# Optimization experiments

Measured on AMD Instinct MI355X. Metric: run time of the kernel, lower is better.

## Reference

```python
import jax, jax.numpy as jnp
import numpy as np

D_MODEL = 1024
NUM_HEADS = 16
D_FF = 4096
EPS = 1e-5


def setup_inputs() -> dict:
    key = jax.random.key(0)
    ks = jax.random.split(key, 8)
    B, S, D = 4, 2048, D_MODEL
    s = 1.0 / np.sqrt(D)
    return {
        "x": jax.random.normal(ks[0], (B, S, D), jnp.float32),
        "ln1_w": jnp.ones((D,), jnp.float32),
        "ln2_w": jnp.ones((D,), jnp.float32),
        "wq": jax.random.normal(ks[1], (D, D), jnp.float32) * s,
        "wk": jax.random.normal(ks[2], (D, D), jnp.float32) * s,
        "wv": jax.random.normal(ks[3], (D, D), jnp.float32) * s,
        "wo": jax.random.normal(ks[4], (D, D), jnp.float32) * s,
        "w1": jax.random.normal(ks[5], (D_FF, D), jnp.float32) * s,
        "w2": jax.random.normal(ks[6], (D, D_FF), jnp.float32) * (1.0 / np.sqrt(D_FF)),
    }


def rmsnorm(a, w):
    # (a * w) / sqrt(mean(a^2) + eps)  -- matches torch module exactly
    denom = jnp.sqrt(jnp.mean(jnp.square(a), axis=-1, keepdims=True) + EPS)
    return a * w / denom


def attention(x, wq, wk, wv, wo):
    B, S, D = x.shape
    H, dk = NUM_HEADS, D // NUM_HEADS
    q = (x @ wq.T).reshape(B, S, H, dk).transpose(0, 2, 1, 3)  # B H S dk
    k = (x @ wk.T).reshape(B, S, H, dk).transpose(0, 2, 1, 3)
    v = (x @ wv.T).reshape(B, S, H, dk).transpose(0, 2, 1, 3)
    scores = jnp.einsum("bhqd,bhkd->bhqk", q, k) / np.sqrt(dk)
    causal = jnp.triu(jnp.ones((S, S), bool), k=1)
    scores = jnp.where(causal, -jnp.inf, scores)
    probs = jax.nn.softmax(scores, axis=-1)
    out = jnp.einsum("bhqk,bhkd->bhqd", probs, v)
    out = out.transpose(0, 2, 1, 3).reshape(B, S, D)
    return out @ wo.T


def ffn(x, w1, w2):
    h = x @ w1.T
    h = 0.5 * h * (1.0 + jax.lax.erf(h / np.sqrt(2.0).astype(np.float32)))
    return h @ w2.T


def reference(x, ln1_w, ln2_w, wq, wk, wv, wo, w1, w2):
    y = x + attention(rmsnorm(x, ln1_w), wq, wk, wv, wo)
    return y + ffn(rmsnorm(y, ln2_w), w1, w2)
```

## Files before the change

### kernel.cpp

```cpp
#include <hip/hip_runtime.h>

#define DM    1024
#define DFF   4096
#define SEQ   2048
#define BATCH 4
#define NROWS (BATCH * SEQ)
#define HEADS 16
#define DKH   64
#define KSTR  (2 * DM)

typedef __attribute__((ext_vector_type(4))) float          f32x4;
typedef __attribute__((ext_vector_type(8))) __bf16         bf16x8;
typedef __attribute__((ext_vector_type(8))) unsigned short u16x8;
typedef __attribute__((ext_vector_type(4))) unsigned short u16x4;

static __device__ __forceinline__ unsigned short f2bf(float f) {
  unsigned u = __builtin_bit_cast(unsigned, f);
  u += 0x7fffu + ((u >> 16) & 1u);
  return (unsigned short)(u >> 16);
}

__global__ void k_f2bf(const float* __restrict__ in, unsigned short* __restrict__ out, int n4) {
  int i = blockIdx.x * blockDim.x + threadIdx.x;
  if (i >= n4) return;
  float4 v = reinterpret_cast<const float4*>(in)[i];
  ushort4 o;
  o.x = f2bf(v.x); o.y = f2bf(v.y); o.z = f2bf(v.z); o.w = f2bf(v.w);
  reinterpret_cast<ushort4*>(out)[i] = o;
}

__global__ __launch_bounds__(256) void k_rmsnorm(const float* __restrict__ x,
                                                 const float* __restrict__ w,
                                                 unsigned short* __restrict__ out) {
  const int row = blockIdx.x;
  const float4 v = reinterpret_cast<const float4*>(x + (size_t)row * DM)[threadIdx.x];
  float ss = v.x * v.x + v.y * v.y + v.z * v.z + v.w * v.w;
#pragma unroll
  for (int off = 32; off > 0; off >>= 1) ss += __shfl_down(ss, off);
  __shared__ float red[4];
  if ((threadIdx.x & 63) == 0) red[threadIdx.x >> 6] = ss;
  __syncthreads();
  const float tot  = red[0] + red[1] + red[2] + red[3];
  const float rden = rsqrtf(tot * (1.0f / DM) + 1e-5f);
  const float4 wv = reinterpret_cast<const float4*>(w)[threadIdx.x];
  ushort4 o;
  o.x = f2bf(v.x * wv.x * rden);
  o.y = f2bf(v.y * wv.y * rden);
  o.z = f2bf(v.z * wv.z * rden);
  o.w = f2bf(v.w * wv.w * rden);
  reinterpret_cast<ushort4*>(out + (size_t)row * DM)[threadIdx.x] = o;
}

template <int EPI>
__global__ __launch_bounds__(256) void k_gemm_nt(const unsigned short* __restrict__ A,
                                                 const unsigned short* __restrict__ B,
                                                 void* __restrict__ Cv,
                                                 const float* __restrict__ res,
                                                 int M, int N, int K) {
  alignas(16) __shared__ unsigned short As[2][128 * 32];
  alignas(16) __shared__ unsigned short Bs[2][128 * 32];
  const int t  = threadIdx.x;
  const int w  = t >> 6;
  const int l  = t & 63;
  const int wr = w >> 1, wc = w & 1;
  const int lr = l & 15, lk = l >> 4;

  const unsigned bid = blockIdx.y * gridDim.x + blockIdx.x;
  const unsigned cpx = (gridDim.x * gridDim.y) >> 3;
  const unsigned sw  = (bid & 7) * cpx + (bid >> 3);
  const int m0 = (int)(sw / gridDim.x) * 128;
  const int n0 = (int)(sw % gridDim.x) * 128;

  const int srow = t >> 2;
  const int sgr  = (t & 3) ^ (srow & 3);

  auto stage = [&](int buf, int k0) {
#pragma unroll
    for (int r = 0; r < 2; ++r) {
      const unsigned short* ga = A + (size_t)(m0 + r * 64 + srow) * K + k0 + 8 * sgr;
      const unsigned short* gb = B + (size_t)(n0 + r * 64 + srow) * K + k0 + 8 * sgr;
      __builtin_amdgcn_global_load_lds((__attribute__((address_space(1))) void*)ga,
                                       (__attribute__((address_space(3))) void*)(&As[buf][r * 2048 + w * 512]),
                                       16, 0, 0);
      __builtin_amdgcn_global_load_lds((__attribute__((address_space(1))) void*)gb,
                                       (__attribute__((address_space(3))) void*)(&Bs[buf][r * 2048 + w * 512]),
                                       16, 0, 0);
    }
  };

  f32x4 acc[4][4] = {};

  stage(0, 0);
  const int nIt = K >> 5;
  for (int it = 0; it < nIt; ++it) {
    const int buf = it & 1;
    __syncthreads();
    if (it + 1 < nIt) stage(buf ^ 1, (it + 1) << 5);

    bf16x8 af[4], bf[4];
#pragma unroll
    for (int m = 0; m < 4; ++m)
      af[m] = *reinterpret_cast<const bf16x8*>(
          &As[buf][(wr * 64 + m * 16 + lr) * 32 + 8 * (lk ^ (lr & 3))]);
#pragma unroll
    for (int n = 0; n < 4; ++n)
      bf[n] = *reinterpret_cast<const bf16x8*>(
          &Bs[buf][(wc * 64 + n * 16 + lr) * 32 + 8 * (lk ^ (lr & 3))]);
#pragma unroll
    for (int m = 0; m < 4; ++m)
#pragma unroll
      for (int n = 0; n < 4; ++n)
        acc[m][n] = __builtin_amdgcn_mfma_f32_16x16x32_bf16(af[m], bf[n], acc[m][n], 0, 0, 0);
  }

#pragma unroll
  for (int m = 0; m < 4; ++m) {
#pragma unroll
    for (int n = 0; n < 4; ++n) {
#pragma unroll
      for (int r = 0; r < 4; ++r) {
        const size_t row = (size_t)(m0 + wr * 64 + m * 16 + lk * 4 + r);
        const size_t col = (size_t)(n0 + wc * 64 + n * 16 + lr);
        const float a = acc[m][n][r];
        if constexpr (EPI == 0) {
          ((unsigned short*)Cv)[row * N + col] = f2bf(a);
        } else if constexpr (EPI == 1) {
          ((float*)Cv)[row * N + col] = a + res[row * N + col];
        } else {
          const float h2 = a * a;
          const float e  = exp2f(a * (2.30221535f + 0.10295355f * h2));
          const float g  = a - a / (e + 1.0f);
          ((unsigned short*)Cv)[row * N + col] = f2bf(g);
        }
      }
    }
  }
}

__global__ __launch_bounds__(256, 2) void k_attn(const unsigned short* __restrict__ QK,
                                                 const unsigned short* __restrict__ VT,
                                                 unsigned short* __restrict__ O) {
  const int qtA = blockIdx.y & 7;
  const int qtB = (int)(SEQ / 128) - 1 - qtA;
  const int h   = blockIdx.x + 8 * (blockIdx.y >> 3);
  const int b   = blockIdx.z;
  const int t  = threadIdx.x, w = t >> 6, l = t & 63;
  const int lr = l & 15, lk = l >> 4;
  const size_t rowB = (size_t)b * SEQ;
  const int hoff  = h * DKH;
  const int qw2[2] = { qtA * 128 + 32 * w, qtB * 128 + 32 * w };

  alignas(16) __shared__ unsigned short Ks[2][64 * 64];
  alignas(16) __shared__ unsigned short Vt[2][64 * 64];
  alignas(16) __shared__ unsigned short Ps[2][4][32 * 64];

  char* const KsB = (char*)Ks;
  char* const VtB = (char*)Vt;

  auto stage = [&](int buf, int kb2) {
#pragma unroll
    for (int half = 0; half < 2; ++half) {
      const int srow = w * 16 + half * 8 + (l >> 3);
      const int sgr  = (l & 7) ^ (srow & 7);
      const unsigned short* gk = QK + (size_t)(rowB + kb2 + srow) * KSTR + DM + hoff + 8 * sgr;
      __builtin_amdgcn_global_load_lds((__attribute__((address_space(1))) void*)gk,
                                       (__attribute__((address_space(3))) void*)(KsB + buf * 8192 + w * 2048 + half * 1024),
                                       16, 0, 0);
      const unsigned short* gv = VT + (size_t)(hoff + srow) * NROWS + rowB + kb2 + 8 * sgr;
      __builtin_amdgcn_global_load_lds((__attribute__((address_space(1))) void*)gv,
                                       (__attribute__((address_space(3))) void*)(VtB + buf * 8192 + w * 2048 + half * 1024),
                                       16, 0, 0);
    }
  };

  bf16x8 qf[2][2][2];
#pragma unroll
  for (int s = 0; s < 2; ++s)
#pragma unroll
    for (int g = 0; g < 2; ++g)
#pragma unroll
      for (int kk = 0; kk < 2; ++kk)
        qf[s][g][kk] = *reinterpret_cast<const bf16x8*>(
            QK + (rowB + qw2[s] + 16 * g + lr) * KSTR + hoff + 32 * kk + 8 * lk);

  f32x4 oacc[2][2][4] = {};
  float mrun[2][2] = {{-1e30f, -1e30f}, {-1e30f, -1e30f}};
  float lrun[2][2] = {{0.0f, 0.0f}, {0.0f, 0.0f}};

  const float SCL = 0.18033688011f;

  const int ktmax = (qtB * 128 + 127) >> 6;
  stage(0, 0);
  for (int kt = 0; kt <= ktmax; ++kt) {
    const int kbase = kt * 64;
    const int cur   = kt & 1;
    __syncthreads();
    if (kt < ktmax) stage(cur ^ 1, kbase + 64);
    const char* Kc = KsB + cur * 8192;
    const char* Vc = VtB + cur * 8192;

    const bool act[2] = { kbase <= qw2[0] + 31, kbase <= qw2[1] + 31 };

    f32x4 sacc[2][2][4] = {};
#pragma unroll
    for (int tt = 0; tt < 4; ++tt) {
      bf16x8 kf0 = *reinterpret_cast<const bf16x8*>(Kc + (16 * tt + lr) * 128 + 16 * ((lk + 0) ^ (lr & 7)));
      bf16x8 kf1 = *reinterpret_cast<const bf16x8*>(Kc + (16 * tt + lr) * 128 + 16 * ((lk + 4) ^ (lr & 7)));
#pragma unroll
      for (int s = 0; s < 2; ++s) {
        if (!act[s]) continue;
#pragma unroll
        for (int g = 0; g < 2; ++g) {
          sacc[s][g][tt] = __builtin_amdgcn_mfma_f32_16x16x32_bf16(kf0, qf[s][g][0], sacc[s][g][tt], 0, 0, 0);
          sacc[s][g][tt] = __builtin_amdgcn_mfma_f32_16x16x32_bf16(kf1, qf[s][g][1], sacc[s][g][tt], 0, 0, 0);
        }
      }
    }

#pragma unroll
    for (int s = 0; s < 2; ++s) {
      if (!act[s]) continue;
      const int qw = qw2[s];
      char* const PsSB = (char*)(Ps[s][w]);
#pragma unroll
      for (int g = 0; g < 2; ++g) {
        const int qg = qw + 16 * g + lr;
        float sv[4][4];
        if (kbase + 63 > qw + 16 * g) {
#pragma unroll
          for (int tt = 0; tt < 4; ++tt)
#pragma unroll
            for (int r = 0; r < 4; ++r) {
              const int kg = kbase + 16 * tt + 4 * lk + r;
              sv[tt][r] = (kg > qg) ? -1e30f : sacc[s][g][tt][r] * SCL;
            }
        } else {
#pragma unroll
          for (int tt = 0; tt < 4; ++tt)
#pragma unroll
            for (int r = 0; r < 4; ++r) sv[tt][r] = sacc[s][g][tt][r] * SCL;
        }
        float tm = sv[0][0];
#pragma unroll
        for (int tt = 0; tt < 4; ++tt)
#pragma unroll
          for (int r = 0; r < 4; ++r) tm = fmaxf(tm, sv[tt][r]);
        tm = fmaxf(tm, __shfl_xor(tm, 16));
        tm = fmaxf(tm, __shfl_xor(tm, 32));
        float mref = mrun[s][g];
        if (__any(tm > mref + 8.0f)) {
          const float mnew  = fmaxf(mref, tm);
          const float alpha = exp2f(mref - mnew);
#pragma unroll
          for (int r = 0; r < 4; ++r) {
            const float ar = __shfl(alpha, 4 * lk + r);
#pragma unroll
            for (int dn = 0; dn < 4; ++dn) oacc[s][g][dn][r] *= ar;
          }
          lrun[s][g] *= alpha;
          mrun[s][g] = mnew;
          mref = mnew;
        }
        float ts = 0.0f;
        unsigned short pb[4][4];
#pragma unroll
        for (int tt = 0; tt < 4; ++tt)
#pragma unroll
          for (int r = 0; r < 4; ++r) {
            const float p = exp2f(sv[tt][r] - mref);
            ts += p;
            pb[tt][r] = __builtin_bit_cast(unsigned short, static_cast<__bf16>(p));
          }
        ts += __shfl_xor(ts, 16);
        ts += __shfl_xor(ts, 32);
        lrun[s][g] += ts;
#pragma unroll
        for (int tt = 0; tt < 4; ++tt) {
          u16x4 pw = {pb[tt][0], pb[tt][1], pb[tt][2], pb[tt][3]};
          *reinterpret_cast<u16x4*>(
              PsSB + (16 * g + lr) * 128 + ((32 * tt + 8 * lk) ^ (16 * (lr & 7)))) = pw;
        }
      }
    }

    asm volatile("" ::: "memory");

#pragma unroll
    for (int kk = 0; kk < 2; ++kk) {
      bf16x8 vf[4];
#pragma unroll
      for (int dn = 0; dn < 4; ++dn)
        vf[dn] = *reinterpret_cast<const bf16x8*>(
            Vc + (16 * dn + lr) * 128 + 16 * ((4 * kk + lk) ^ (lr & 7)));
#pragma unroll
      for (int s = 0; s < 2; ++s) {
        if (!act[s]) continue;
        char* const PsSB = (char*)(Ps[s][w]);
        bf16x8 pa[2];
#pragma unroll
        for (int g = 0; g < 2; ++g)
          pa[g] = *reinterpret_cast<const bf16x8*>(
              PsSB + (16 * g + lr) * 128 + ((64 * kk + 16 * lk) ^ (16 * (lr & 7))));
#pragma unroll
        for (int dn = 0; dn < 4; ++dn) {
          oacc[s][0][dn] = __builtin_amdgcn_mfma_f32_16x16x32_bf16(pa[0], vf[dn], oacc[s][0][dn], 0, 0, 0);
          oacc[s][1][dn] = __builtin_amdgcn_mfma_f32_16x16x32_bf16(pa[1], vf[dn], oacc[s][1][dn], 0, 0, 0);
        }
      }
    }

    asm volatile("" ::: "memory");
  }

#pragma unroll
  for (int s = 0; s < 2; ++s)
#pragma unroll
    for (int g = 0; g < 2; ++g)
#pragma unroll
      for (int r = 0; r < 4; ++r) {
        const float li = 1.0f / __shfl(lrun[s][g], 4 * lk + r);
        const size_t row = rowB + qw2[s] + 16 * g + 4 * lk + r;
#pragma unroll
        for (int dn = 0; dn < 4; ++dn)
          O[row * DM + hoff + 16 * dn + lr] = f2bf(oacc[s][g][dn][r] * li);
      }
}

extern "C" void kernel_launch(void* const* d_in, const int* in_sizes, int n_in,
                              void* d_out, int out_size, void* d_ws, size_t ws_size,
                              hipStream_t stream) {
  const float* x   = (const float*)d_in[0];
  const float* ln1 = (const float*)d_in[1];
  const float* ln2 = (const float*)d_in[2];
  const float* wq  = (const float*)d_in[3];
  const float* wk  = (const float*)d_in[4];
  const float* wv  = (const float*)d_in[5];
  const float* wo  = (const float*)d_in[6];
  const float* w1  = (const float*)d_in[7];
  const float* w2  = (const float*)d_in[8];

  char* ws = (char*)d_ws;
  size_t off = 0;
  auto take = [&](size_t bytes) { void* p = ws + off; off += bytes; return p; };
  unsigned short* wqkb = (unsigned short*)take((size_t)2 * DM * DM * 2);
  unsigned short* wvb  = (unsigned short*)take((size_t)DM * DM * 2);
  unsigned short* wob  = (unsigned short*)take((size_t)DM * DM * 2);
  unsigned short* w1b  = (unsigned short*)take((size_t)DFF * DM * 2);
  unsigned short* w2b  = (unsigned short*)take((size_t)DM * DFF * 2);
  unsigned short* qk   = (unsigned short*)take((size_t)NROWS * 2 * DM * 2);
  unsigned short* xn   = (unsigned short*)take((size_t)NROWS * DM * 2);
  unsigned short* vtb  = (unsigned short*)take((size_t)DM * NROWS * 2);
  float*          yb   = (float*)take((size_t)NROWS * DM * 4);
  unsigned short* hb   = (unsigned short*)take((size_t)NROWS * DFF * 2);
  unsigned short* yn   = qk;

  auto cvt = [&](const float* src, unsigned short* dst, size_t n) {
    int n4 = (int)(n / 4);
    k_f2bf<<<dim3((n4 + 255) / 256), dim3(256), 0, stream>>>(src, dst, n4);
  };
  cvt(wq, wqkb, (size_t)DM * DM);
  cvt(wk, wqkb + (size_t)DM * DM, (size_t)DM * DM);
  cvt(wv, wvb, (size_t)DM * DM);
  cvt(wo, wob, (size_t)DM * DM);
  cvt(w1, w1b, (size_t)DFF * DM);
  cvt(w2, w2b, (size_t)DM * DFF);

  k_rmsnorm<<<dim3(NROWS), dim3(256), 0, stream>>>(x, ln1, xn);

  k_gemm_nt<0><<<dim3(2 * DM / 128, NROWS / 128), dim3(256), 0, stream>>>(
      xn, wqkb, qk, nullptr, NROWS, 2 * DM, DM);

  k_gemm_nt<0><<<dim3(NROWS / 128, DM / 128), dim3(256), 0, stream>>>(
      wvb, xn, vtb, nullptr, DM, NROWS, DM);

  k_attn<<<dim3(SEQ / 256, HEADS, BATCH), dim3(256), 0, stream>>>(qk, vtb, xn);

  const dim3 gD(DM / 128, NROWS / 128);
  k_gemm_nt<1><<<gD, dim3(256), 0, stream>>>(xn, wob, yb, x, NROWS, DM, DM);

  k_rmsnorm<<<dim3(NROWS), dim3(256), 0, stream>>>(yb, ln2, yn);

  k_gemm_nt<2><<<dim3(DFF / 128, NROWS / 128), dim3(256), 0, stream>>>(yn, w1b, hb, nullptr, NROWS, DFF, DM);
  k_gemm_nt<1><<<gD, dim3(256), 0, stream>>>(hb, w2b, (float*)d_out, yb, NROWS, DM, DFF);
}
```

Before: 434.5 us.

## Halve attention query tile per wave and fold softmax scale into Q projection

The attention kernel now gives each wave 16 query rows per tile instead of 32, using 64-row tile pairs. This doubles the grid to 16x16x4 blocks and raises launch bounds to 3 blocks per CU, for more parallelism and finer causal load balance. The softmax scale (1/sqrt(dk)·log2e) is folded into the Q half of the QK projection epilogue, which removes a multiply per score. In exchange, each K/V tile staged in shared memory is reused by fewer queries, so K/V global traffic rises. Q is also rounded to bf16 after scaling, which slightly changes numerics.

```diff
diff --git a/kernel.cpp b/kernel.cpp
--- a/kernel.cpp
+++ b/kernel.cpp
@@ -126,33 +126,36 @@
           ((unsigned short*)Cv)[row * N + col] = f2bf(a);
         } else if constexpr (EPI == 1) {
           ((float*)Cv)[row * N + col] = a + res[row * N + col];
-        } else {
+        } else if constexpr (EPI == 2) {
           const float h2 = a * a;
           const float e  = exp2f(a * (2.30221535f + 0.10295355f * h2));
           const float g  = a - a / (e + 1.0f);
           ((unsigned short*)Cv)[row * N + col] = f2bf(g);
+        } else {
+          const float sc = (col < DM) ? 0.18033688011f : 1.0f;
+          ((unsigned short*)Cv)[row * N + col] = f2bf(a * sc);
         }
       }
     }
   }
 }
 
-__global__ __launch_bounds__(256, 2) void k_attn(const unsigned short* __restrict__ QK,
+__global__ __launch_bounds__(256, 3) void k_attn(const unsigned short* __restrict__ QK,
                                                  const unsigned short* __restrict__ VT,
                                                  unsigned short* __restrict__ O) {
-  const int qtA = blockIdx.y & 7;
-  const int qtB = (int)(SEQ / 128) - 1 - qtA;
-  const int h   = blockIdx.x + 8 * (blockIdx.y >> 3);
+  const int h   = blockIdx.x;
+  const int qtA = blockIdx.y;
+  const int qtB = 31 - qtA;
   const int b   = blockIdx.z;
   const int t  = threadIdx.x, w = t >> 6, l = t & 63;
   const int lr = l & 15, lk = l >> 4;
   const size_t rowB = (size_t)b * SEQ;
   const int hoff  = h * DKH;
-  const int qw2[2] = { qtA * 128 + 32 * w, qtB * 128 + 32 * w };
+  const int qw2[2] = { qtA * 64 + 16 * w, qtB * 64 + 16 * w };
 
   alignas(16) __shared__ unsigned short Ks[2][64 * 64];
   alignas(16) __shared__ unsigned short Vt[2][64 * 64];
-  alignas(16) __shared__ unsigned short Ps[2][4][32 * 64];
+  alignas(16) __shared__ unsigned short Ps[2][4][16 * 64];
 
   char* const KsB = (char*)Ks;
   char* const VtB = (char*)Vt;
@@ -173,23 +176,19 @@
     }
   };
 
-  bf16x8 qf[2][2][2];
+  bf16x8 qf[2][2];
 #pragma unroll
   for (int s = 0; s < 2; ++s)
 #pragma unroll
-    for (int g = 0; g < 2; ++g)
-#pragma unroll
-      for (int kk = 0; kk < 2; ++kk)
-        qf[s][g][kk] = *reinterpret_cast<const bf16x8*>(
-            QK + (rowB + qw2[s] + 16 * g + lr) * KSTR + hoff + 32 * kk + 8 * lk);
-
-  f32x4 oacc[2][2][4] = {};
-  float mrun[2][2] = {{-1e30f, -1e30f}, {-1e30f, -1e30f}};
-  float lrun[2][2] = {{0.0f, 0.0f}, {0.0f, 0.0f}};
-
-  const float SCL = 0.18033688011f;
-
-  const int ktmax = (qtB * 128 + 127) >> 6;
+    for (int kk = 0; kk < 2; ++kk)
+      qf[s][kk] = *reinterpret_cast<const bf16x8*>(
+          QK + (rowB + qw2[s] + lr) * KSTR + hoff + 32 * kk + 8 * lk);
+
+  f32x4 oacc[2][4] = {};
+  float mrun[2] = {-1e30f, -1e30f};
+  float lrun[2] = {0.0f, 0.0f};
+
+  const int ktmax = qtB;
   stage(0, 0);
   for (int kt = 0; kt <= ktmax; ++kt) {
     const int kbase = kt * 64;
@@ -199,9 +198,9 @@
     const char* Kc = KsB + cur * 8192;
     const char* Vc = VtB + cur * 8192;
 
-    const bool act[2] = { kbase <= qw2[0] + 31, kbase <= qw2[1] + 31 };
-
-    f32x4 sacc[2][2][4] = {};
+    const bool act[2] = { kbase <= qw2[0] + 15, kbase <= qw2[1] + 15 };
+
+    f32x4 sacc[2][4] = {};
 #pragma unroll
     for (int tt = 0; tt < 4; ++tt) {
       bf16x8 kf0 = *reinterpret_cast<const bf16x8*>(Kc + (16 * tt + lr) * 128 + 16 * ((lk + 0) ^ (lr & 7)));
@@ -209,11 +208,8 @@
 #pragma unroll
       for (int s = 0; s < 2; ++s) {
         if (!act[s]) continue;
-#pragma unroll
-        for (int g = 0; g < 2; ++g) {
-          sacc[s][g][tt] = __builtin_amdgcn_mfma_f32_16x16x32_bf16(kf0, qf[s][g][0], sacc[s][g][tt], 0, 0, 0);
-          sacc[s][g][tt] = __builtin_amdgcn_mfma_f32_16x16x32_bf16(kf1, qf[s][g][1], sacc[s][g][tt], 0, 0, 0);
-        }
+        sacc[s][tt] = __builtin_amdgcn_mfma_f32_16x16x32_bf16(kf0, qf[s][0], sacc[s][tt], 0, 0, 0);
+        sacc[s][tt] = __builtin_amdgcn_mfma_f32_16x16x32_bf16(kf1, qf[s][1], sacc[s][tt], 0, 0, 0);
       }
     }
 
@@ -222,64 +218,61 @@
       if (!act[s]) continue;
       const int qw = qw2[s];
       char* const PsSB = (char*)(Ps[s][w]);
-#pragma unroll
-      for (int g = 0; g < 2; ++g) {
-        const int qg = qw + 16 * g + lr;
-        float sv[4][4];
-        if (kbase + 63 > qw + 16 * g) {
-#pragma unroll
-          for (int tt = 0; tt < 4; ++tt)
-#pragma unroll
-            for (int r = 0; r < 4; ++r) {
-              const int kg = kbase + 16 * tt + 4 * lk + r;
-              sv[tt][r] = (kg > qg) ? -1e30f : sacc[s][g][tt][r] * SCL;
-            }
-        } else {
-#pragma unroll
-          for (int tt = 0; tt < 4; ++tt)
-#pragma unroll
-            for (int r = 0; r < 4; ++r) sv[tt][r] = sacc[s][g][tt][r] * SCL;
+      const int qg = qw + lr;
+      float sv[4][4];
+      if (kbase + 63 > qw) {
+#pragma unroll
+        for (int tt = 0; tt < 4; ++tt)
+#pragma unroll
+          for (int r = 0; r < 4; ++r) {
+            const int kg = kbase + 16 * tt + 4 * lk + r;
+            sv[tt][r] = (kg > qg) ? -1e30f : sacc[s][tt][r];
+          }
+      } else {
+#pragma unroll
+        for (int tt = 0; tt < 4; ++tt)
+#pragma unroll
+          for (int r = 0; r < 4; ++r) sv[tt][r] = sacc[s][tt][r];
+      }
+      float tm = sv[0][0];
+#pragma unroll
+      for (int tt = 0; tt < 4; ++tt)
+#pragma unroll
+        for (int r = 0; r < 4; ++r) tm = fmaxf(tm, sv[tt][r]);
+      tm = fmaxf(tm, __shfl_xor(tm, 16));
+      tm = fmaxf(tm, __shfl_xor(tm, 32));
+      float mref = mrun[s];
+      if (__any(tm > mref + 8.0f)) {
+        const float mnew  = fmaxf(mref, tm);
+        const float alpha = exp2f(mref - mnew);
+#pragma unroll
+        for (int r = 0; r < 4; ++r) {
+          const float ar = __shfl(alpha, 4 * lk + r);
+#pragma unroll
+          for (int dn = 0; dn < 4; ++dn) oacc[s][dn][r] *= ar;
         }
-        float tm = sv[0][0];
-#pragma unroll
-        for (int tt = 0; tt < 4; ++tt)
-#pragma unroll
-          for (int r = 0; r < 4; ++r) tm = fmaxf(tm, sv[tt][r]);
-        tm = fmaxf(tm, __shfl_xor(tm, 16));
-        tm = fmaxf(tm, __shfl_xor(tm, 32));
-        float mref = mrun[s][g];
-        if (__any(tm > mref + 8.0f)) {
-          const float mnew  = fmaxf(mref, tm);
-          const float alpha = exp2f(mref - mnew);
-#pragma unroll
-          for (int r = 0; r < 4; ++r) {
-            const float ar = __shfl(alpha, 4 * lk + r);
-#pragma unroll
-            for (int dn = 0; dn < 4; ++dn) oacc[s][g][dn][r] *= ar;
-          }
-          lrun[s][g] *= alpha;
-          mrun[s][g] = mnew;
-          mref = mnew;
+        lrun[s] *= alpha;
+        mrun[s] = mnew;
+        mref = mnew;
+      }
+      float ts = 0.0f;
+      unsigned short pb[4][4];
+#pragma unroll
+      for (int tt = 0; tt < 4; ++tt)
+#pragma unroll
+        for (int r = 0; r < 4; ++r) {
+          const float p = exp2f(sv[tt][r] - mref);
+          ts += p;
+          pb[tt][r] = __builtin_bit_cast(unsigned short, static_cast<__bf16>(p));
         }
-        float ts = 0.0f;
-        unsigned short pb[4][4];
-#pragma unroll
-        for (int tt = 0; tt < 4; ++tt)
-#pragma unroll
-          for (int r = 0; r < 4; ++r) {
-            const float p = exp2f(sv[tt][r] - mref);
-            ts += p;
-            pb[tt][r] = __builtin_bit_cast(unsigned short, static_cast<__bf16>(p));
-          }
-        ts += __shfl_xor(ts, 16);
-        ts += __shfl_xor(ts, 32);
-        lrun[s][g] += ts;
-#pragma unroll
-        for (int tt = 0; tt < 4; ++tt) {
-          u16x4 pw = {pb[tt][0], pb[tt][1], pb[tt][2], pb[tt][3]};
-          *reinterpret_cast<u16x4*>(
-              PsSB + (16 * g + lr) * 128 + ((32 * tt + 8 * lk) ^ (16 * (lr & 7)))) = pw;
-        }
+      ts += __shfl_xor(ts, 16);
+      ts += __shfl_xor(ts, 32);
+      lrun[s] += ts;
+#pragma unroll
+      for (int tt = 0; tt < 4; ++tt) {
+        u16x4 pw = {pb[tt][0], pb[tt][1], pb[tt][2], pb[tt][3]};
+        *reinterpret_cast<u16x4*>(
+            PsSB + lr * 128 + ((32 * tt + 8 * lk) ^ (16 * (lr & 7)))) = pw;
       }
     }
 
@@ -296,16 +289,11 @@
       for (int s = 0; s < 2; ++s) {
         if (!act[s]) continue;
         char* const PsSB = (char*)(Ps[s][w]);
-        bf16x8 pa[2];
-#pragma unroll
-        for (int g = 0; g < 2; ++g)
-          pa[g] = *reinterpret_cast<const bf16x8*>(
-              PsSB + (16 * g + lr) * 128 + ((64 * kk + 16 * lk) ^ (16 * (lr & 7))));
-#pragma unroll
-        for (int dn = 0; dn < 4; ++dn) {
-          oacc[s][0][dn] = __builtin_amdgcn_mfma_f32_16x16x32_bf16(pa[0], vf[dn], oacc[s][0][dn], 0, 0, 0);
-          oacc[s][1][dn] = __builtin_amdgcn_mfma_f32_16x16x32_bf16(pa[1], vf[dn], oacc[s][1][dn], 0, 0, 0);
-        }
+        bf16x8 pa = *reinterpret_cast<const bf16x8*>(
+            PsSB + lr * 128 + ((64 * kk + 16 * lk) ^ (16 * (lr & 7))));
+#pragma unroll
+        for (int dn = 0; dn < 4; ++dn)
+          oacc[s][dn] = __builtin_amdgcn_mfma_f32_16x16x32_bf16(pa, vf[dn], oacc[s][dn], 0, 0, 0);
       }
     }
 
@@ -315,15 +303,13 @@
 #pragma unroll
   for (int s = 0; s < 2; ++s)
 #pragma unroll
-    for (int g = 0; g < 2; ++g)
-#pragma unroll
-      for (int r = 0; r < 4; ++r) {
-        const float li = 1.0f / __shfl(lrun[s][g], 4 * lk + r);
-        const size_t row = rowB + qw2[s] + 16 * g + 4 * lk + r;
-#pragma unroll
-        for (int dn = 0; dn < 4; ++dn)
-          O[row * DM + hoff + 16 * dn + lr] = f2bf(oacc[s][g][dn][r] * li);
-      }
+    for (int r = 0; r < 4; ++r) {
+      const float li = 1.0f / __shfl(lrun[s], 4 * lk + r);
+      const size_t row = rowB + qw2[s] + 4 * lk + r;
+#pragma unroll
+      for (int dn = 0; dn < 4; ++dn)
+        O[row * DM + hoff + 16 * dn + lr] = f2bf(oacc[s][dn][r] * li);
+    }
 }
 
 extern "C" void kernel_launch(void* const* d_in, const int* in_sizes, int n_in,
@@ -367,13 +353,13 @@
 
   k_rmsnorm<<<dim3(NROWS), dim3(256), 0, stream>>>(x, ln1, xn);
 
-  k_gemm_nt<0><<<dim3(2 * DM / 128, NROWS / 128), dim3(256), 0, stream>>>(
+  k_gemm_nt<3><<<dim3(2 * DM / 128, NROWS / 128), dim3(256), 0, stream>>>(
       xn, wqkb, qk, nullptr, NROWS, 2 * DM, DM);
 
   k_gemm_nt<0><<<dim3(NROWS / 128, DM / 128), dim3(256), 0, stream>>>(
       wvb, xn, vtb, nullptr, DM, NROWS, DM);
 
-  k_attn<<<dim3(SEQ / 256, HEADS, BATCH), dim3(256), 0, stream>>>(qk, vtb, xn);
+  k_attn<<<dim3(HEADS, 16, BATCH), dim3(256), 0, stream>>>(qk, vtb, xn);
 
   const dim3 gD(DM / 128, NROWS / 128);
   k_gemm_nt<1><<<gD, dim3(256), 0, stream>>>(xn, wob, yb, x, NROWS, DM, DM);
```

New measurement: 438.4 us. About the same (+0.9%).
